# Optimization experiments

Measured on AMD Instinct MI355X. Metric: run time of the kernel, lower is better.

## Reference

```python
import jax, jax.numpy as jnp
import numpy as np

N = 50000      # nodes
E = 500000     # edges
IN_FEAT = 128
OUT_FEAT = 128
R = 200        # num_relations
NB = 16        # num_bases -> 8x8 blocks
SI = IN_FEAT // NB   # submat_in = 8
SO = OUT_FEAT // NB  # submat_out = 8


def setup_inputs() -> dict:
    key = jax.random.key(0)
    k1, k2, k3, k4, k5, k6, k7 = jax.random.split(key, 7)
    h = jax.random.normal(k1, (N, IN_FEAT), dtype=jnp.float32)
    norm = jax.random.uniform(k2, (N, 1), dtype=jnp.float32)
    weight = jax.random.normal(k3, (R, NB * SI * SO), dtype=jnp.float32) * 0.1
    loop_weight = jax.random.normal(k4, (IN_FEAT, OUT_FEAT), dtype=jnp.float32) * 0.1
    src = jax.random.randint(k5, (E,), 0, N, dtype=jnp.int32)
    dst = jax.random.randint(k6, (E,), 0, N, dtype=jnp.int32)
    etype = jax.random.randint(k7, (E,), 0, R, dtype=jnp.int32)
    return {"h": h, "norm": norm, "weight": weight, "loop_weight": loop_weight,
            "src": src, "dst": dst, "etype": etype}


def reference(h, norm, weight, loop_weight, src, dst, etype):
    # self-loop message: [N, out_feat]
    loop_message = h @ loop_weight
    # per-edge relation-weight gather: [E, NB, SI, SO]
    w_e = weight[etype].reshape(-1, NB, SI, SO)
    # src features as per-basis blocks: [E, NB, SI]
    x_e = h[src].reshape(-1, NB, SI)
    # block-diagonal bmm -> messages [E, out_feat]
    msg = jnp.einsum('ebi,ebio->ebo', x_e, w_e).reshape(-1, OUT_FEAT)
    # scatter-sum to destination nodes (fn.sum(msg -> h))
    agg = jax.ops.segment_sum(msg, dst, num_segments=N)
    # apply_func: multiply by per-node norm, then add self-loop and activation
    nodes = agg * norm
    nodes = nodes + loop_message
    return jax.nn.relu(nodes)
```

## Files before the change

kernel.cpp:

```cpp
#include <hip/hip_runtime.h>
#include <hip/hip_bf16.h>


#define IN_FEAT 128
#define OUT_FEAT 128
#define SCAN_CHUNK 512

using short8  = __attribute__((ext_vector_type(8))) short;
using float4v = __attribute__((ext_vector_type(4))) float;

__device__ inline float blo(unsigned u) { return __uint_as_float(u << 16); }
__device__ inline float bhi(unsigned u) { return __uint_as_float(u & 0xffff0000u); }
__device__ inline unsigned short f2bf(float f) {
  __hip_bfloat16 b = __float2bfloat16(f);
  return *reinterpret_cast<unsigned short*>(&b);
}

__device__ inline float dot2bf(unsigned x, unsigned w, float c) {
#if __has_builtin(__builtin_amdgcn_fdot2_f32_bf16)
  typedef __bf16 bf16x2 __attribute__((ext_vector_type(2)));
  return __builtin_amdgcn_fdot2_f32_bf16(__builtin_bit_cast(bf16x2, x),
                                         __builtin_bit_cast(bf16x2, w), c, false);
#else
  return c + blo(x) * blo(w) + bhi(x) * bhi(w);
#endif
}

__global__ __launch_bounds__(256) void k_prep(
    const float* __restrict__ w, unsigned short* __restrict__ w16, int wtotal,
    const float* __restrict__ h, uint4* __restrict__ h16p, int htotal8,
    const float* __restrict__ lw, unsigned short* __restrict__ lwT,
    const int* __restrict__ dst, int* __restrict__ cnt, int E,
    int bw, int bh, int blw) {
  const int bid = blockIdx.x;
  if (bid < bw) {
    const int idx = bid * 256 + threadIdx.x;
    if (idx < wtotal) {
      const int r = idx >> 10;
      const int rem = idx & 1023;
      const int b = rem >> 6;
      const int q = rem & 63;
      const int opp = q >> 4;
      const int t = q & 15;
      const int j = t >> 3;
      const int i = t & 7;
      w16[idx] = f2bf(w[((size_t)r << 10) + b * 64 + i * 8 + opp * 2 + j]);
    }
  } else if (bid < bw + bh) {
    const int t = (bid - bw) * 256 + threadIdx.x;
    if (t < htotal8) {
      const float4 a = ((const float4*)h)[2 * t];
      const float4 b = ((const float4*)h)[2 * t + 1];
      uint4 o;
      o.x = (unsigned)f2bf(a.x) | ((unsigned)f2bf(a.y) << 16);
      o.y = (unsigned)f2bf(a.z) | ((unsigned)f2bf(a.w) << 16);
      o.z = (unsigned)f2bf(b.x) | ((unsigned)f2bf(b.y) << 16);
      o.w = (unsigned)f2bf(b.z) | ((unsigned)f2bf(b.w) << 16);
      h16p[t] = o;
    }
  } else if (bid < bw + bh + blw) {
    const int idx = (bid - bw - bh) * 256 + threadIdx.x;
    if (idx < IN_FEAT * OUT_FEAT) {
      const int o = idx >> 7;
      const int k = idx & 127;
      lwT[idx] = f2bf(lw[k * 128 + o]);
    }
  } else {
    const int e = (bid - bw - bh - blw) * 256 + threadIdx.x;
    if (e < E) atomicAdd(&cnt[dst[e]], 1);
  }
}

__global__ __launch_bounds__(256) void k_gemm_sum(
    const unsigned short* __restrict__ h16, const unsigned short* __restrict__ lwT,
    float* __restrict__ out, int N,
    const int* __restrict__ cnt, int* __restrict__ bsum, int gemm_blocks) {
  if (blockIdx.x < gemm_blocks) {
    const int wid = threadIdx.x >> 6;
    const int lane = threadIdx.x & 63;
    const int row0 = blockIdx.x * 64 + wid * 16;
    if (row0 >= N) return;
    const int m = lane & 15;
    const int kg = (lane >> 4) * 8;
    const int arow = min(row0 + m, N - 1);

    float4v acc[8];
    #pragma unroll
    for (int nt = 0; nt < 8; ++nt) acc[nt] = (float4v){0.f, 0.f, 0.f, 0.f};

    const unsigned short* ap = h16 + (size_t)arow * 128 + kg;
    const unsigned short* bp = lwT + (size_t)m * 128 + kg;

    #pragma unroll
    for (int kc = 0; kc < 4; ++kc) {
      const short8 a = *(const short8*)(ap + kc * 32);
      #pragma unroll
      for (int nt = 0; nt < 8; ++nt) {
        const short8 b = *(const short8*)(bp + nt * 2048 + kc * 32);
        acc[nt] = __builtin_amdgcn_mfma_f32_16x16x32_bf16(a, b, acc[nt], 0, 0, 0);
      }
    }

    const int crow = row0 + (lane >> 4) * 4;
    #pragma unroll
    for (int nt = 0; nt < 8; ++nt) {
      #pragma unroll
      for (int r = 0; r < 4; ++r) {
        const int row = crow + r;
        if (row < N) out[(size_t)row * 128 + nt * 16 + m] = acc[nt][r];
      }
    }
  } else {
    __shared__ int s[256];
    const int cb = blockIdx.x - gemm_blocks;
    const int t = threadIdx.x;
    const int base = cb * SCAN_CHUNK;
    int v = 0;
    const int i0 = base + t, i1 = base + 256 + t;
    if (i0 < N) v += cnt[i0];
    if (i1 < N) v += cnt[i1];
    s[t] = v;
    __syncthreads();
    for (int d = 128; d > 0; d >>= 1) {
      if (t < d) s[t] += s[t + d];
      __syncthreads();
    }
    if (t == 0) bsum[cb] = s[0];
  }
}

__global__ __launch_bounds__(256) void k_chunksum(
    const int* __restrict__ cnt, int* __restrict__ bsum, int N) {
  __shared__ int s[256];
  const int t = threadIdx.x;
  const int base = blockIdx.x * SCAN_CHUNK;
  int v = 0;
  int i0 = base + t, i1 = base + 256 + t;
  if (i0 < N) v += cnt[i0];
  if (i1 < N) v += cnt[i1];
  s[t] = v;
  __syncthreads();
  for (int d = 128; d > 0; d >>= 1) {
    if (t < d) s[t] += s[t + d];
    __syncthreads();
  }
  if (t == 0) bsum[blockIdx.x] = s[0];
}

__global__ __launch_bounds__(256) void k_hist(
    const int* __restrict__ dst, int* __restrict__ cnt, int E) {
  const int e = blockIdx.x * blockDim.x + threadIdx.x;
  if (e < E) atomicAdd(&cnt[dst[e]], 1);
}

__global__ __launch_bounds__(256) void k_offsets(
    const int* __restrict__ cnt, const int* __restrict__ bsum,
    int* __restrict__ pos, int N) {
  __shared__ int s[256];
  __shared__ int sbase;
  const int t = threadIdx.x;
  if (t < 64) {
    int acc = 0;
    for (int j = t; j < (int)blockIdx.x; j += 64) acc += bsum[j];
    #pragma unroll
    for (int d = 1; d < 64; d <<= 1) acc += __shfl_xor(acc, d);
    if (t == 0) sbase = acc;
  }
  const int base = blockIdx.x * SCAN_CHUNK;
  const int i0 = base + 2 * t;
  const int i1 = i0 + 1;
  const int c0 = (i0 < N) ? cnt[i0] : 0;
  const int c1 = (i1 < N) ? cnt[i1] : 0;
  const int pair = c0 + c1;
  s[t] = pair;
  __syncthreads();
  #pragma unroll
  for (int d = 1; d < 256; d <<= 1) {
    int v = (t >= d) ? s[t - d] : 0;
    __syncthreads();
    s[t] += v;
    __syncthreads();
  }
  const int ex = s[t] - pair + sbase;
  if (i0 < N) pos[i0] = ex;
  if (i1 < N) pos[i1] = ex + c0;
}

__global__ __launch_bounds__(256) void k_scatter(
    const int* __restrict__ src, const int* __restrict__ dst,
    const int* __restrict__ etype, int* __restrict__ pos,
    int2* __restrict__ srcet, int E) {
  const int e = blockIdx.x * blockDim.x + threadIdx.x;
  if (e < E) {
    const int p = atomicAdd(&pos[dst[e]], 1);
    srcet[p] = make_int2(src[e], etype[e]);
  }
}

__global__ __launch_bounds__(256) void agg_bf16_2w(
    const unsigned short* __restrict__ h16, const float* __restrict__ norm,
    const unsigned short* __restrict__ w16, const int* __restrict__ pos,
    const int* __restrict__ cnt, const int2* __restrict__ srcet,
    float* __restrict__ out, int N) {
  __shared__ float red[2][128];
  const int wid = threadIdx.x >> 6;
  const int lane = threadIdx.x & 63;
  const int sub = wid >> 1;
  const int half = wid & 1;
  const int node = blockIdx.x * 2 + sub;

  const int b = lane >> 2;
  const int opp = lane & 3;
  const int woff = b * 64 + opp * 16;
  const int hoff = b * 8;
  const int o = b * 8 + opp * 2;

  float a0 = 0.f, a1 = 0.f;
  if (node < N) {
    const int num = cnt[node];
    const int end = pos[node];
    const int begin = end - num;
    for (int base = 0; base < num; base += 64) {
      const int cn = min(64, num - base);
      const int2 my = srcet[begin + base + min(lane, cn - 1)];
      #pragma unroll 2
      for (int i = half; i < cn; i += 2) {
        const int s = __shfl(my.x, i);
        const int r = __shfl(my.y, i);
        const unsigned short* wp = w16 + ((size_t)r << 10) + woff;
        const uint4 wa = *(const uint4*)(wp);
        const uint4 wb = *(const uint4*)(wp + 8);
        const uint4 xv = *(const uint4*)(h16 + ((size_t)s << 7) + hoff);

        a0 = dot2bf(xv.x, wa.x, a0);
        a0 = dot2bf(xv.y, wa.y, a0);
        a0 = dot2bf(xv.z, wa.z, a0);
        a0 = dot2bf(xv.w, wa.w, a0);
        a1 = dot2bf(xv.x, wb.x, a1);
        a1 = dot2bf(xv.y, wb.y, a1);
        a1 = dot2bf(xv.z, wb.z, a1);
        a1 = dot2bf(xv.w, wb.w, a1);
      }
    }
  }

  if (half == 1) {
    *(float2*)&red[sub][o] = make_float2(a0, a1);
  }
  __syncthreads();
  if (half == 0 && node < N) {
    const float2 other = *(const float2*)&red[sub][o];
    const float nm = norm[node];
    float* outp = out + ((size_t)node << 7) + o;
    const float2 prev = *(const float2*)outp;
    float2 res;
    res.x = fmaxf(prev.x + (a0 + other.x) * nm, 0.f);
    res.y = fmaxf(prev.y + (a1 + other.y) * nm, 0.f);
    *(float2*)outp = res;
  }
}

__global__ __launch_bounds__(256) void selfloop_gemm(
    const float* __restrict__ h, const float* __restrict__ lw,
    float* __restrict__ out, int n) {
  __shared__ float slw[IN_FEAT * OUT_FEAT];
  __shared__ float sh[32 * IN_FEAT];

  {
    const float4* s4 = (const float4*)lw;
    float4* d4 = (float4*)slw;
    for (int i = threadIdx.x; i < IN_FEAT * OUT_FEAT / 4; i += 256) d4[i] = s4[i];
  }

  const int cg = threadIdx.x & 31;
  const int rg = threadIdx.x >> 5;

  for (int base = blockIdx.x * 32; base < n; base += gridDim.x * 32) {
    const int nrows = min(32, n - base);
    __syncthreads();
    {
      const float4* hs = (const float4*)(h + (size_t)base * IN_FEAT);
      float4* sd = (float4*)sh;
      const int cnt = nrows * (IN_FEAT / 4);
      for (int i = threadIdx.x; i < cnt; i += 256) sd[i] = hs[i];
    }
    __syncthreads();

    float4 acc[4];
    #pragma unroll
    for (int j = 0; j < 4; ++j) acc[j] = make_float4(0.f, 0.f, 0.f, 0.f);

    #pragma unroll 4
    for (int k = 0; k < IN_FEAT; ++k) {
      const float4 w = ((const float4*)slw)[k * 32 + cg];
      #pragma unroll
      for (int j = 0; j < 4; ++j) {
        const float hv = sh[(rg + 8 * j) * IN_FEAT + k];
        acc[j].x += hv * w.x;
        acc[j].y += hv * w.y;
        acc[j].z += hv * w.z;
        acc[j].w += hv * w.w;
      }
    }

    #pragma unroll
    for (int j = 0; j < 4; ++j) {
      const int r = rg + 8 * j;
      if (r < nrows) {
        ((float4*)(out + (size_t)(base + r) * OUT_FEAT))[cg] = acc[j];
      }
    }
  }
}

__global__ __launch_bounds__(256) void agg(
    const float* __restrict__ h, const float* __restrict__ norm,
    const float* __restrict__ weight, const int* __restrict__ pos,
    const int* __restrict__ cnt, const int2* __restrict__ srcet,
    float* __restrict__ out, int N) {
  const int node = (int)((blockIdx.x * blockDim.x + threadIdx.x) >> 6);
  const int lane = threadIdx.x & 63;
  if (node >= N) return;

  const int b = lane >> 2;
  const int op = (lane & 3) * 2;
  const int boff = b * 64 + op;

  const int num = cnt[node];
  const int end = pos[node];
  const int begin = end - num;

  float a0 = 0.f, a1 = 0.f;

  for (int base = 0; base < num; base += 64) {
    const int cn = min(64, num - base);
    const int2 my = srcet[begin + base + min(lane, cn - 1)];
    #pragma unroll 2
    for (int i = 0; i < cn; ++i) {
      const int s = __shfl(my.x, i);
      const int r = __shfl(my.y, i);
      const float* xp = h + ((size_t)s << 7) + b * 8;
      const float4 x0 = ((const float4*)xp)[0];
      const float4 x1 = ((const float4*)xp)[1];
      const float* wp = weight + ((size_t)r << 10) + boff;
      const float2 w0 = *(const float2*)(wp);
      const float2 w1 = *(const float2*)(wp + 8);
      const float2 w2 = *(const float2*)(wp + 16);
      const float2 w3 = *(const float2*)(wp + 24);
      const float2 w4 = *(const float2*)(wp + 32);
      const float2 w5 = *(const float2*)(wp + 40);
      const float2 w6 = *(const float2*)(wp + 48);
      const float2 w7 = *(const float2*)(wp + 56);
      a0 += x0.x * w0.x; a1 += x0.x * w0.y;
      a0 += x0.y * w1.x; a1 += x0.y * w1.y;
      a0 += x0.z * w2.x; a1 += x0.z * w2.y;
      a0 += x0.w * w3.x; a1 += x0.w * w3.y;
      a0 += x1.x * w4.x; a1 += x1.x * w4.y;
      a0 += x1.y * w5.x; a1 += x1.y * w5.y;
      a0 += x1.z * w6.x; a1 += x1.z * w6.y;
      a0 += x1.w * w7.x; a1 += x1.w * w7.y;
    }
  }

  const float nm = norm[node];
  const int o = b * 8 + op;
  float* outp = out + ((size_t)node << 7) + o;
  float2 prev = *(const float2*)outp;
  float2 res;
  res.x = fmaxf(prev.x + a0 * nm, 0.f);
  res.y = fmaxf(prev.y + a1 * nm, 0.f);
  *(float2*)outp = res;
}

__global__ __launch_bounds__(256) void edge_msg(
    const float* __restrict__ h, const float* __restrict__ norm,
    const float* __restrict__ weight, const int* __restrict__ src,
    const int* __restrict__ dst, const int* __restrict__ etype,
    float* out, int E) {
  const int wave = (int)((blockIdx.x * blockDim.x + threadIdx.x) >> 6);
  const int lane = threadIdx.x & 63;
  if (wave >= E) return;

  const int s = src[wave];
  const int d = dst[wave];
  const int r = etype[wave];
  const float nrm = norm[d];

  const int b = lane >> 2;
  const int op = (lane & 3) * 2;

  const float* xp = h + (size_t)s * IN_FEAT + b * 8;
  const float4 x0 = ((const float4*)xp)[0];
  const float4 x1 = ((const float4*)xp)[1];
  float x[8] = {x0.x, x0.y, x0.z, x0.w, x1.x, x1.y, x1.z, x1.w};

  const float* wp = weight + (size_t)r * 1024 + b * 64 + op;
  float a0 = 0.f, a1 = 0.f;
  #pragma unroll
  for (int i = 0; i < 8; ++i) {
    const float2 w = *(const float2*)(wp + i * 8);
    a0 += x[i] * w.x;
    a1 += x[i] * w.y;
  }

  const int o = b * 8 + op;
  float* outp = out + (size_t)d * OUT_FEAT + o;
  atomicAdd(outp, a0 * nrm);
  atomicAdd(outp + 1, a1 * nrm);
}

__global__ __launch_bounds__(256) void relu_k(float* __restrict__ out, int n4) {
  const int i = blockIdx.x * blockDim.x + threadIdx.x;
  if (i < n4) {
    float4 v = ((const float4*)out)[i];
    v.x = fmaxf(v.x, 0.f);
    v.y = fmaxf(v.y, 0.f);
    v.z = fmaxf(v.z, 0.f);
    v.w = fmaxf(v.w, 0.f);
    ((float4*)out)[i] = v;
  }
}

extern "C" void kernel_launch(void* const* d_in, const int* in_sizes, int n_in,
                              void* d_out, int out_size, void* d_ws, size_t ws_size,
                              hipStream_t stream) {
  const float* h    = (const float*)d_in[0];
  const float* norm = (const float*)d_in[1];
  const float* w    = (const float*)d_in[2];
  const float* lw   = (const float*)d_in[3];
  const int* src    = (const int*)d_in[4];
  const int* dst    = (const int*)d_in[5];
  const int* etype  = (const int*)d_in[6];
  float* out = (float*)d_out;

  const int N = in_sizes[1];
  const int E = in_sizes[4];
  const int R = in_sizes[2] / 1024;
  const int nblk = (N + SCAN_CHUNK - 1) / SCAN_CHUNK;

  const size_t nb_bsum = (size_t)((nblk < 128) ? 128 : nblk);
  const size_t off_cnt  = (size_t)E * 8;
  const size_t off_pos  = off_cnt + (size_t)N * 4;
  const size_t off_bsum = off_pos + (size_t)N * 4;
  size_t off_h16 = off_bsum + nb_bsum * 4;
  off_h16 = (off_h16 + 15) & ~(size_t)15;
  const size_t off_w16 = off_h16 + (size_t)N * IN_FEAT * 2;
  const size_t off_lwT = off_w16 + (size_t)R * 1024 * 2;
  const size_t need_full = off_lwT + (size_t)IN_FEAT * OUT_FEAT * 2;
  const size_t need_sort = off_bsum + nb_bsum * 4;

  if (ws_size >= need_full) {
    char* wsb = (char*)d_ws;
    int2* srcet = (int2*)wsb;
    int* cnt  = (int*)(wsb + off_cnt);
    int* pos  = (int*)(wsb + off_pos);
    int* bsum = (int*)(wsb + off_bsum);
    unsigned short* h16 = (unsigned short*)(wsb + off_h16);
    unsigned short* w16 = (unsigned short*)(wsb + off_w16);
    unsigned short* lwT = (unsigned short*)(wsb + off_lwT);

    hipMemsetAsync(cnt, 0, (size_t)N * 4, stream);

    const int wtotal = R * 1024;
    const int htotal8 = N * IN_FEAT / 8;
    const int bw  = (wtotal + 255) / 256;
    const int bh  = (htotal8 + 255) / 256;
    const int blw = (IN_FEAT * OUT_FEAT + 255) / 256;
    const int bhist = (E + 255) / 256;
    k_prep<<<bw + bh + blw + bhist, 256, 0, stream>>>(
        w, w16, wtotal, h, (uint4*)h16, htotal8, lw, lwT, dst, cnt, E,
        bw, bh, blw);

    const int gemm_blocks = (N + 63) / 64;
    k_gemm_sum<<<gemm_blocks + nblk, 256, 0, stream>>>(
        h16, lwT, out, N, cnt, bsum, gemm_blocks);

    k_offsets<<<nblk, 256, 0, stream>>>(cnt, bsum, pos, N);
    k_scatter<<<(E + 255) / 256, 256, 0, stream>>>(src, dst, etype, pos, srcet, E);

    agg_bf16_2w<<<(N + 1) / 2, 256, 0, stream>>>(h16, norm, w16, pos, cnt,
                                                 srcet, out, N);
  } else if (ws_size >= need_sort) {
    char* wsb = (char*)d_ws;
    int2* srcet = (int2*)wsb;
    int* cnt  = (int*)(wsb + off_cnt);
    int* pos  = (int*)(wsb + off_pos);
    int* bsum = (int*)(wsb + off_bsum);

    selfloop_gemm<<<512, 256, 0, stream>>>(h, lw, out, N);
    hipMemsetAsync(cnt, 0, (size_t)N * 4, stream);
    k_hist<<<(E + 255) / 256, 256, 0, stream>>>(dst, cnt, E);
    k_chunksum<<<nblk, 256, 0, stream>>>(cnt, bsum, N);
    k_offsets<<<nblk, 256, 0, stream>>>(cnt, bsum, pos, N);
    k_scatter<<<(E + 255) / 256, 256, 0, stream>>>(src, dst, etype, pos, srcet, E);
    agg<<<(N + 3) / 4, 256, 0, stream>>>(h, norm, w, pos, cnt, srcet, out, N);
  } else {
    selfloop_gemm<<<512, 256, 0, stream>>>(h, lw, out, N);
    edge_msg<<<(E + 3) / 4, 256, 0, stream>>>(h, norm, w, src, dst, etype, out, E);
    const int n4 = N * OUT_FEAT / 4;
    relu_k<<<(n4 + 255) / 256, 256, 0, stream>>>(out, n4);
  }
}
```

Measured before the change: 152.2 us.

## Vectorize histogram/scatter edges and use one wave per node in aggregation

The histogram and scatter kernels now have each thread handle four edges through int4 loads, with the grid shrunk to match. The aggregation kernel changes from two waves per node combined through an LDS reduction and a block barrier to a single wave per node, with four nodes per block. It also switches its gathers to nontemporal loads. This removes the shared-memory reduction and the sync, but halves the parallelism per node and could hurt L2 reuse of the weights and features because of the nontemporal hints.

```diff
diff --git a/kernel.cpp b/kernel.cpp
--- a/kernel.cpp
+++ b/kernel.cpp
@@ -8,6 +8,8 @@
 
 using short8  = __attribute__((ext_vector_type(8))) short;
 using float4v = __attribute__((ext_vector_type(4))) float;
+using uintx4  = __attribute__((ext_vector_type(4))) unsigned;
+using intx2   = __attribute__((ext_vector_type(2))) int;
 
 __device__ inline float blo(unsigned u) { return __uint_as_float(u << 16); }
 __device__ inline float bhi(unsigned u) { return __uint_as_float(u & 0xffff0000u); }
@@ -66,8 +68,16 @@
       lwT[idx] = f2bf(lw[k * 128 + o]);
     }
   } else {
-    const int e = (bid - bw - bh - blw) * 256 + threadIdx.x;
-    if (e < E) atomicAdd(&cnt[dst[e]], 1);
+    const int e0 = ((bid - bw - bh - blw) * 256 + threadIdx.x) * 4;
+    if (e0 + 3 < E) {
+      const int4 d4 = *(const int4*)(dst + e0);
+      atomicAdd(&cnt[d4.x], 1);
+      atomicAdd(&cnt[d4.y], 1);
+      atomicAdd(&cnt[d4.z], 1);
+      atomicAdd(&cnt[d4.w], 1);
+    } else {
+      for (int e = e0; e < E; ++e) atomicAdd(&cnt[dst[e]], 1);
+    }
   }
 }
 
@@ -190,74 +200,77 @@
     const int* __restrict__ src, const int* __restrict__ dst,
     const int* __restrict__ etype, int* __restrict__ pos,
     int2* __restrict__ srcet, int E) {
-  const int e = blockIdx.x * blockDim.x + threadIdx.x;
-  if (e < E) {
-    const int p = atomicAdd(&pos[dst[e]], 1);
-    srcet[p] = make_int2(src[e], etype[e]);
-  }
-}
-
-__global__ __launch_bounds__(256) void agg_bf16_2w(
+  const int e0 = (blockIdx.x * blockDim.x + threadIdx.x) * 4;
+  if (e0 + 3 < E) {
+    const int4 s4 = *(const int4*)(src + e0);
+    const int4 d4 = *(const int4*)(dst + e0);
+    const int4 t4 = *(const int4*)(etype + e0);
+    int p;
+    p = atomicAdd(&pos[d4.x], 1); srcet[p] = make_int2(s4.x, t4.x);
+    p = atomicAdd(&pos[d4.y], 1); srcet[p] = make_int2(s4.y, t4.y);
+    p = atomicAdd(&pos[d4.z], 1); srcet[p] = make_int2(s4.z, t4.z);
+    p = atomicAdd(&pos[d4.w], 1); srcet[p] = make_int2(s4.w, t4.w);
+  } else {
+    for (int e = e0; e < E; ++e) {
+      const int p = atomicAdd(&pos[dst[e]], 1);
+      srcet[p] = make_int2(src[e], etype[e]);
+    }
+  }
+}
+
+__global__ __launch_bounds__(256) void agg_bf16(
     const unsigned short* __restrict__ h16, const float* __restrict__ norm,
     const unsigned short* __restrict__ w16, const int* __restrict__ pos,
     const int* __restrict__ cnt, const int2* __restrict__ srcet,
     float* __restrict__ out, int N) {
-  __shared__ float red[2][128];
-  const int wid = threadIdx.x >> 6;
+  const int node = (int)((blockIdx.x * blockDim.x + threadIdx.x) >> 6);
   const int lane = threadIdx.x & 63;
-  const int sub = wid >> 1;
-  const int half = wid & 1;
-  const int node = blockIdx.x * 2 + sub;
+  if (node >= N) return;
 
   const int b = lane >> 2;
   const int opp = lane & 3;
   const int woff = b * 64 + opp * 16;
   const int hoff = b * 8;
+
+  const int num = cnt[node];
+  const int end = pos[node];
+  const int begin = end - num;
+
+  float a0 = 0.f, a1 = 0.f;
+
+  for (int base = 0; base < num; base += 64) {
+    const int cn = min(64, num - base);
+    const intx2 my = __builtin_nontemporal_load(
+        (const intx2*)(srcet + begin + base + min(lane, cn - 1)));
+    #pragma unroll 4
+    for (int i = 0; i < cn; ++i) {
+      const int s = __shfl(my[0], i);
+      const int r = __shfl(my[1], i);
+      const unsigned short* wp = w16 + ((size_t)r << 10) + woff;
+      const uintx4 wa = __builtin_nontemporal_load((const uintx4*)wp);
+      const uintx4 wb = __builtin_nontemporal_load((const uintx4*)(wp + 8));
+      const uintx4 xv = __builtin_nontemporal_load(
+          (const uintx4*)(h16 + ((size_t)s << 7) + hoff));
+
+      a0 = dot2bf(xv[0], wa[0], a0);
+      a0 = dot2bf(xv[1], wa[1], a0);
+      a0 = dot2bf(xv[2], wa[2], a0);
+      a0 = dot2bf(xv[3], wa[3], a0);
+      a1 = dot2bf(xv[0], wb[0], a1);
+      a1 = dot2bf(xv[1], wb[1], a1);
+      a1 = dot2bf(xv[2], wb[2], a1);
+      a1 = dot2bf(xv[3], wb[3], a1);
+    }
+  }
+
+  const float nm = norm[node];
   const int o = b * 8 + opp * 2;
-
-  float a0 = 0.f, a1 = 0.f;
-  if (node < N) {
-    const int num = cnt[node];
-    const int end = pos[node];
-    const int begin = end - num;
-    for (int base = 0; base < num; base += 64) {
-      const int cn = min(64, num - base);
-      const int2 my = srcet[begin + base + min(lane, cn - 1)];
-      #pragma unroll 2
-      for (int i = half; i < cn; i += 2) {
-        const int s = __shfl(my.x, i);
-        const int r = __shfl(my.y, i);
-        const unsigned short* wp = w16 + ((size_t)r << 10) + woff;
-        const uint4 wa = *(const uint4*)(wp);
-        const uint4 wb = *(const uint4*)(wp + 8);
-        const uint4 xv = *(const uint4*)(h16 + ((size_t)s << 7) + hoff);
-
-        a0 = dot2bf(xv.x, wa.x, a0);
-        a0 = dot2bf(xv.y, wa.y, a0);
-        a0 = dot2bf(xv.z, wa.z, a0);
-        a0 = dot2bf(xv.w, wa.w, a0);
-        a1 = dot2bf(xv.x, wb.x, a1);
-        a1 = dot2bf(xv.y, wb.y, a1);
-        a1 = dot2bf(xv.z, wb.z, a1);
-        a1 = dot2bf(xv.w, wb.w, a1);
-      }
-    }
-  }
-
-  if (half == 1) {
-    *(float2*)&red[sub][o] = make_float2(a0, a1);
-  }
-  __syncthreads();
-  if (half == 0 && node < N) {
-    const float2 other = *(const float2*)&red[sub][o];
-    const float nm = norm[node];
-    float* outp = out + ((size_t)node << 7) + o;
-    const float2 prev = *(const float2*)outp;
-    float2 res;
-    res.x = fmaxf(prev.x + (a0 + other.x) * nm, 0.f);
-    res.y = fmaxf(prev.y + (a1 + other.y) * nm, 0.f);
-    *(float2*)outp = res;
-  }
+  float* outp = out + ((size_t)node << 7) + o;
+  float2 prev = *(const float2*)outp;
+  float2 res;
+  res.x = fmaxf(prev.x + a0 * nm, 0.f);
+  res.y = fmaxf(prev.y + a1 * nm, 0.f);
+  *(float2*)outp = res;
 }
 
 __global__ __launch_bounds__(256) void selfloop_gemm(
@@ -466,7 +479,7 @@
     const int bw  = (wtotal + 255) / 256;
     const int bh  = (htotal8 + 255) / 256;
     const int blw = (IN_FEAT * OUT_FEAT + 255) / 256;
-    const int bhist = (E + 255) / 256;
+    const int bhist = (E + 1023) / 1024;
     k_prep<<<bw + bh + blw + bhist, 256, 0, stream>>>(
         w, w16, wtotal, h, (uint4*)h16, htotal8, lw, lwT, dst, cnt, E,
         bw, bh, blw);
@@ -476,10 +489,11 @@
         h16, lwT, out, N, cnt, bsum, gemm_blocks);
 
     k_offsets<<<nblk, 256, 0, stream>>>(cnt, bsum, pos, N);
-    k_scatter<<<(E + 255) / 256, 256, 0, stream>>>(src, dst, etype, pos, srcet, E);
-
-    agg_bf16_2w<<<(N + 1) / 2, 256, 0, stream>>>(h16, norm, w16, pos, cnt,
-                                                 srcet, out, N);
+    k_scatter<<<(E + 1023) / 1024, 256, 0, stream>>>(src, dst, etype, pos,
+                                                     srcet, E);
+
+    agg_bf16<<<(N + 3) / 4, 256, 0, stream>>>(h16, norm, w16, pos, cnt, srcet,
+                                              out, N);
   } else if (ws_size >= need_sort) {
     char* wsb = (char*)d_ws;
     int2* srcet = (int2*)wsb;
@@ -492,7 +506,8 @@
     k_hist<<<(E + 255) / 256, 256, 0, stream>>>(dst, cnt, E);
     k_chunksum<<<nblk, 256, 0, stream>>>(cnt, bsum, N);
     k_offsets<<<nblk, 256, 0, stream>>>(cnt, bsum, pos, N);
-    k_scatter<<<(E + 255) / 256, 256, 0, stream>>>(src, dst, etype, pos, srcet, E);
+    k_scatter<<<(E + 1023) / 1024, 256, 0, stream>>>(src, dst, etype, pos,
+                                                     srcet, E);
     agg<<<(N + 3) / 4, 256, 0, stream>>>(h, norm, w, pos, cnt, srcet, out, N);
   } else {
     selfloop_gemm<<<512, 256, 0, stream>>>(h, lw, out, N);
```

Result: slower. 229.6 us (+50.9%).
